# Performance work log

Hardware: AMD Instinct MI355X
Metric: run time of the kernel (lower is better)

The kernel has to match this reference:

```python
import jax, jax.numpy as jnp
import numpy as np

B, T, E, H = 8, 2048, 1024, 128


def setup_inputs() -> dict:
    key = jax.random.key(0)
    kx, kk, kq, kv = jax.random.split(key, 4)
    x = jax.random.normal(kx, (B, T, E), dtype=jnp.float32)
    # nn.Linear(E, H, bias=False) weights, stored as (E, H) so y = x @ W
    scale = 0.02
    Wk = jax.random.normal(kk, (E, H), dtype=jnp.float32) * scale
    Wq = jax.random.normal(kq, (E, H), dtype=jnp.float32) * scale
    Wv = jax.random.normal(kv, (E, H), dtype=jnp.float32) * scale
    return {"x": x, "Wk": Wk, "Wq": Wq, "Wv": Wv}


def reference(x, Wk, Wq, Wv):
    # x: (B,T,E) -> k,q,v: (B,T,H)
    k = x @ Wk
    q = x @ Wq
    v = x @ Wv
    # att[b,t,s] = q[b,t] . k[b,s]
    att = jnp.einsum('bth,bsh->bts', q, k)
    # original: att / head_norm, head_norm = 1/sqrt(H)  => multiply by sqrt(H)
    att = att * jnp.sqrt(jnp.float32(H))
    tril = jnp.tril(jnp.ones((T, T), dtype=bool))
    att = jnp.where(tril, att, -jnp.inf)
    # original softmax over dim=1 (query axis), NOT the key axis
    att = jax.nn.softmax(att, axis=1)
    return att @ v  # (B,T,H)
```

## Files before the change

### kernel.cpp

```cpp
#include <hip/hip_runtime.h>
#include <math.h>

#define Bn 8
#define Tn 2048
#define En 1024
#define Hn 128
#define SQRTH_LOG2E (11.313708498984761f * 1.4426950408889634f)

typedef __attribute__((ext_vector_type(8))) short short8;
typedef __attribute__((ext_vector_type(8))) _Float16 half8;
typedef __attribute__((ext_vector_type(4))) short short4v;
typedef __attribute__((ext_vector_type(4))) float float4v;

#define MFMA16(a, b, c)  __builtin_amdgcn_mfma_f32_16x16x32_bf16((a), (b), (c), 0, 0, 0)
#define MFMA16F(a, b, c) __builtin_amdgcn_mfma_f32_16x16x32_f16((a), (b), (c), 0, 0, 0)
#define EXP2(x) __builtin_amdgcn_exp2f(x)

static __device__ __forceinline__ unsigned short f2bf(float f) {
    unsigned u = __float_as_uint(f);
    u += 0x7FFFu + ((u >> 16) & 1u);
    return (unsigned short)(u >> 16);
}
static __device__ __forceinline__ unsigned short f2h(float f) {
    _Float16 h = (_Float16)f;
    union { _Float16 v; unsigned short u; } c; c.v = h; return c.u;
}

static __device__ __forceinline__ void gll16(const unsigned short* g, unsigned short* l) {
    __builtin_amdgcn_global_load_lds(
        (const __attribute__((address_space(1))) unsigned int*)g,
        (__attribute__((address_space(3))) unsigned int*)l, 16, 0, 0);
}


__global__ __launch_bounds__(256) void prep_kernel(
    const float* __restrict__ x,
    const float* __restrict__ Wq, const float* __restrict__ Wk, const float* __restrict__ Wv,
    unsigned short* __restrict__ xt, unsigned short* __restrict__ wtt)
{
    if (blockIdx.x < 8192) {
        int g = blockIdx.x * 256 + threadIdx.x;
        int kc8 = g & 3;
        int rr = (g >> 2) & 63;
        int ks = (g >> 8) & 31;
        int mt = g >> 13;
        size_t src = ((size_t)mt * 64 + rr) * En + ks * 32 + kc8 * 8;
        float4v f0 = *(const float4v*)(x + src);
        float4v f1 = *(const float4v*)(x + src + 4);
        short8 h;
#pragma unroll
        for (int j = 0; j < 4; j++) {
            h[j] = (short)f2h(f0[j]);
            h[j + 4] = (short)f2h(f1[j]);
        }
        size_t d = (size_t)(g >> 2) * 32 + (size_t)(kc8 ^ (rr & 3)) * 8;
        *(short8*)(xt + d) = h;
    } else {
        int t = (blockIdx.x - 8192) * 256 + threadIdx.x;
        int kc8 = t & 3;
        int hh = (t >> 2) & 127;
        int ks = (t >> 9) & 31;
        int z = t >> 14;
        const float* W = (z == 0) ? Wq : ((z == 1) ? Wk : Wv);
        short8 h8;
#pragma unroll
        for (int j = 0; j < 8; j++) {
            int e = ks * 32 + kc8 * 8 + j;
            h8[j] = (short)f2h(W[(size_t)e * Hn + hh]);
        }
        size_t d = (((size_t)z * 32 + ks) * 4096) + (size_t)hh * 32
                 + (size_t)(kc8 ^ (hh & 3)) * 8;
        *(short8*)(wtt + d) = h8;
    }
}

__global__ __launch_bounds__(256) void proj_kernel(
    const unsigned short* __restrict__ xt, const unsigned short* __restrict__ wtt,
    unsigned short* __restrict__ qf, unsigned short* __restrict__ kf,
    unsigned short* __restrict__ vtt)
{
    __shared__ __align__(16) unsigned short lds[2][6144];
    int z = blockIdx.y;
    int mt = blockIdx.x;
    int tid = threadIdx.x;
    int wave = tid >> 6, lane = tid & 63;
    int c15 = lane & 15, kg = lane >> 4;
    int sb = c15 & 3;
    int mrow = wave >> 1, ncol = wave & 1;

    const unsigned short* A0 = xt + (size_t)mt * 32 * 2048;
    const unsigned short* B0 = wtt + (size_t)z * 32 * 4096;

    float4v acc[2][4];
#pragma unroll
    for (int i = 0; i < 2; i++)
#pragma unroll
        for (int j = 0; j < 4; j++) acc[i][j] = (float4v)0.0f;

    const unsigned short* gcur[3];
    int lbo[3];
    int gstep[3];
#pragma unroll
    for (int i = 0; i < 3; i++) {
        int ch = wave * 3 + i;
        if (ch < 4) { gcur[i] = A0 + ch * 512;       lbo[i] = ch * 512;        gstep[i] = 2048; }
        else        { gcur[i] = B0 + (ch - 4) * 512; lbo[i] = 2048 + (ch - 4) * 512; gstep[i] = 4096; }
    }
    int lo8 = lane * 8;

    auto stage = [&](int buf) {
        unsigned short* Lb = lds[0] + buf * 6144;
#pragma unroll
        for (int i = 0; i < 3; i++) {
            gll16(gcur[i] + lo8, Lb + lbo[i] + lo8);
            gcur[i] += gstep[i];
        }
    };

    stage(0);

    for (int ks = 0; ks < 32; ks++) {
        __syncthreads();
        if (ks + 1 < 32) stage((ks + 1) & 1);
        const unsigned short* Lb = lds[ks & 1];

        half8 ah[2], bh[4];
#pragma unroll
        for (int mi = 0; mi < 2; mi++) {
            int row = mrow * 32 + mi * 16 + c15;
            ah[mi] = *(const half8*)(Lb + row * 32 + (kg ^ sb) * 8);
        }
#pragma unroll
        for (int ni = 0; ni < 4; ni++) {
            int row = ncol * 64 + ni * 16 + c15;
            bh[ni] = *(const half8*)(Lb + 2048 + row * 32 + (kg ^ sb) * 8);
        }
#pragma unroll
        for (int mi = 0; mi < 2; mi++)
#pragma unroll
            for (int ni = 0; ni < 4; ni++)
                acc[mi][ni] = MFMA16F(ah[mi], bh[ni], acc[mi][ni]);
    }

    if (z < 2) {
        unsigned short* oh = (z == 0) ? qf : kf;
#pragma unroll
        for (int mi = 0; mi < 2; mi++) {
#pragma unroll
            for (int ni = 0; ni < 4; ni++) {
                int h = ncol * 64 + ni * 16 + c15;
#pragma unroll
                for (int r = 0; r < 4; r++) {
                    int t = mt * 64 + mrow * 32 + mi * 16 + kg * 4 + r;
                    size_t o = (size_t)t * Hn + (((h >> 3) ^ (t & 15)) << 3) + (h & 7);
                    oh[o] = f2h(acc[mi][ni][r]);
                }
            }
        }
    } else {
        int b = mt >> 5;
#pragma unroll
        for (int mi = 0; mi < 2; mi++) {
            int t0 = (mt & 31) * 64 + mrow * 32 + mi * 16 + kg * 4;
            int sc = t0 >> 5, so = t0 & 31;
#pragma unroll
            for (int ni = 0; ni < 4; ni++) {
                int h = ncol * 64 + ni * 16 + c15;
                short4v pk;
#pragma unroll
                for (int r = 0; r < 4; r++) pk[r] = (short)f2bf(acc[mi][ni][r]);
                int so2 = ((((so >> 3) ^ ((h >> 1) & 3))) << 3) | (so & 7);
                *(short4v*)(vtt + (((size_t)b * 64 + sc) * 128 + h) * 32 + so2) = pk;
            }
        }
    }
}

__global__ __launch_bounds__(256) void stats_part_kernel(
    const unsigned short* __restrict__ qf, const unsigned short* __restrict__ kf,
    float* __restrict__ m_part, float* __restrict__ l_part)
{
    __shared__ __align__(16) unsigned short lds[4096];
    int tid = threadIdx.x;
    int wave = tid >> 6, lane = tid & 63;
    int c15 = lane & 15, kg = lane >> 4;
    int b = blockIdx.x;

    int rem = (int)blockIdx.y, sj, nch = 1;
    for (sj = 0; sj < 32; sj++) {
        nch = ((31 - sj) >> 2) + 1;
        if (rem < nch) break;
        rem -= nch;
    }
    int ci = rem;
    int c0 = 2 * sj;
    int len = 64 - c0;
    int cbase = len / nch, ext = len % nch;
    int cs = c0 + ci * cbase + (ci < ext ? ci : ext);
    int ce = cs + cbase + (ci < ext ? 1 : 0);

    int s_base = sj * 64 + wave * 16;

    half8 a[4];
    {
        int s = s_base + c15;
        const unsigned short* kr = kf + ((size_t)(b * Tn + s)) * Hn;
#pragma unroll
        for (int st = 0; st < 4; st++) {
            int off = ((st * 4 + kg) ^ c15) * 8;
            a[st] = *(const half8*)(kr + off);
        }
    }
    float m[4], l[4];
#pragma unroll
    for (int r = 0; r < 4; r++) { m[r] = -3.0e38f; l[r] = 0.0f; }

    auto stage = [&](int c) {
        const unsigned short* Qf = qf + ((size_t)b * Tn + c * 32) * Hn;
        int lo8 = lane * 8;
#pragma unroll
        for (int i = 0; i < 2; i++) {
            int ch = wave * 2 + i;
            gll16(Qf + ch * 512 + lo8, lds + ch * 512 + lo8);
        }
    };

    for (int c = cs; c < ce; c++) {
        stage(c);
        __syncthreads();
#pragma unroll
        for (int half = 0; half < 2; half++) {
            int t16 = c * 32 + half * 16;
            int tl = half * 16 + c15;
            float4v a1 = (float4v)0.0f;
#pragma unroll
            for (int st = 0; st < 4; st++) {
                int off = tl * 128 + ((st * 4 + kg) ^ c15) * 8;
                half8 bh = *(const half8*)(lds + off);
                a1 = MFMA16F(a[st], bh, a1);
            }
            int t = t16 + c15;
#pragma unroll
            for (int r = 0; r < 4; r++) {
                float attv = a1[r] * SQRTH_LOG2E;
                int s_row = s_base + kg * 4 + r;
                bool valid = (t >= s_row);
                float cand = valid ? attv : -3.0e38f;
                float mn = fmaxf(m[r], cand);
                l[r] = l[r] * EXP2(m[r] - mn) + (valid ? EXP2(attv - mn) : 0.0f);
                m[r] = mn;
            }
        }
        __syncthreads();
    }
#pragma unroll
    for (int mask = 1; mask < 16; mask <<= 1) {
#pragma unroll
        for (int r = 0; r < 4; r++) {
            float mo = __shfl_xor(m[r], mask);
            float lo2 = __shfl_xor(l[r], mask);
            float mn = fmaxf(m[r], mo);
            l[r] = l[r] * EXP2(m[r] - mn) + lo2 * EXP2(mo - mn);
            m[r] = mn;
        }
    }
    if (c15 == 0) {
#pragma unroll
        for (int r = 0; r < 4; r++) {
            int sl = wave * 16 + kg * 4 + r;
            size_t d = ((((size_t)b * 32 + sj) * 8 + ci) * 64) + sl;
            m_part[d] = m[r];
            l_part[d] = l[r];
        }
    }
}

__global__ __launch_bounds__(256) void stats_combine_kernel(
    const float* __restrict__ m_part, const float* __restrict__ l_part,
    float2* __restrict__ ml_st)
{
    int g = blockIdx.x * 256 + threadIdx.x;
    int s = g & 2047, b = g >> 11;
    int sj = s >> 6, sl = s & 63;
    int nch = ((31 - sj) >> 2) + 1;
    size_t base = (((size_t)b * 32 + sj) * 8) * 64 + sl;
    float M = m_part[base];
    float L = l_part[base];
    for (int ci = 1; ci < nch; ci++) {
        float mi = m_part[base + (size_t)ci * 64];
        float li = l_part[base + (size_t)ci * 64];
        float mn = fmaxf(M, mi);
        L = L * EXP2(M - mn) + li * EXP2(mi - mn);
        M = mn;
    }
    float2 ml; ml.x = M; ml.y = 1.0f / L;
    ml_st[(size_t)b * Tn + s] = ml;
}

__global__ __launch_bounds__(256) void out_part_kernel(
    const unsigned short* __restrict__ qf, const unsigned short* __restrict__ kf,
    const unsigned short* __restrict__ vtt,
    const float2* __restrict__ ml_st,
    float* __restrict__ part_out)
{
    __shared__ __align__(16) unsigned short lds[8192];
    __shared__ __align__(16) unsigned short pbuf[4][16][40];
    int tid = threadIdx.x;
    int wave = tid >> 6, lane = tid & 63;
    int c15 = lane & 15, kg = lane >> 4;
    int b = blockIdx.x;

    int rem = (int)blockIdx.y, tj, nch = 1;
    for (tj = 31; tj >= 0; tj--) {
        nch = (tj >> 2) + 1;
        if (rem < nch) break;
        rem -= nch;
    }
    int ci = rem;
    int len = 2 * tj + 2;
    int cbase = len / nch, ext = len % nch;
    int cs = ci * cbase + (ci < ext ? ci : ext);
    int ce = cs + cbase + (ci < ext ? 1 : 0);

    int t_base = tj * 64 + wave * 16;

    half8 qa[4];
    {
        int t = t_base + c15;
        const unsigned short* qr = qf + ((size_t)(b * Tn + t)) * Hn;
#pragma unroll
        for (int st = 0; st < 4; st++) {
            int off = ((st * 4 + kg) ^ c15) * 8;
            qa[st] = *(const half8*)(qr + off);
        }
    }
    float4v oacc[8];
#pragma unroll
    for (int i = 0; i < 8; i++) oacc[i] = (float4v)0.0f;

    auto stage = [&](int c) {
        const unsigned short* Kf = kf + ((size_t)b * Tn + c * 32) * Hn;
        const unsigned short* Vv = vtt + ((size_t)b * 64 + c) * (128 * 32);
        int lo8 = lane * 8;
#pragma unroll
        for (int i = 0; i < 4; i++) {
            int ch = wave * 4 + i;
            const unsigned short* g;
            unsigned short* ld;
            if (ch < 8) { g = Kf + ch * 512;       ld = lds + ch * 512; }
            else        { g = Vv + (ch - 8) * 512; ld = lds + 4096 + (ch - 8) * 512; }
            gll16(g + lo8, ld + lo8);
        }
    };

    for (int c = cs; c < ce; c++) {
        stage(c);
        __syncthreads();
#pragma unroll
        for (int half = 0; half < 2; half++) {
            int s16 = c * 32 + half * 16;
            int sl = half * 16 + c15;
            float4v a1 = (float4v)0.0f;
#pragma unroll
            for (int st = 0; st < 4; st++) {
                int off = sl * 128 + ((st * 4 + kg) ^ c15) * 8;
                half8 bh = *(const half8*)(lds + off);
                a1 = MFMA16F(qa[st], bh, a1);
            }
            float2 mlv = ml_st[b * Tn + s16 + c15];
#pragma unroll
            for (int r = 0; r < 4; r++) {
                int t = t_base + kg * 4 + r;
                float attv = a1[r] * SQRTH_LOG2E;
                float earg = fminf(attv - mlv.x, 0.0f);
                float p = (t >= s16 + c15) ? EXP2(earg) * mlv.y : 0.0f;
                pbuf[wave][kg * 4 + r][c15 + half * 16] = f2bf(p);
            }
        }
        short8 pa = *(const short8*)&pbuf[wave][c15][kg * 8];
#pragma unroll
        for (int nt = 0; nt < 8; nt++) {
            int voff = (nt * 16 + c15) * 32 + ((kg ^ ((c15 >> 1) & 3)) * 8);
            short8 vb = *(const short8*)(lds + 4096 + voff);
            oacc[nt] = MFMA16(pa, vb, oacc[nt]);
        }
        __syncthreads();
    }
    float* po = part_out + ((((size_t)b * 32 + tj) * 8 + ci) * 64) * 128;
#pragma unroll
    for (int nt = 0; nt < 8; nt++) {
        int h = nt * 16 + c15;
#pragma unroll
        for (int r = 0; r < 4; r++) {
            int tl = wave * 16 + kg * 4 + r;
            po[(size_t)tl * 128 + h] = oacc[nt][r];
        }
    }
}

__global__ __launch_bounds__(256) void out_combine_kernel(
    const float* __restrict__ part_out, float* __restrict__ out)
{
    int g = blockIdx.x * 256 + threadIdx.x;
    int h4 = g & 31;
    int t = (g >> 5) & 2047;
    int b = g >> 16;
    int tj = t >> 6, tl = t & 63;
    int nch = (tj >> 2) + 1;
    const float4v* p = (const float4v*)(part_out
        + ((((size_t)b * 32 + tj) * 8) * 64 + tl) * 128) + h4;
    float4v acc = p[0];
    for (int ci = 1; ci < nch; ci++) acc += p[(size_t)ci * 2048];
    *((float4v*)(out + ((size_t)b * Tn + t) * Hn) + h4) = acc;
}

extern "C" void kernel_launch(void* const* d_in, const int* in_sizes, int n_in,
                              void* d_out, int out_size, void* d_ws, size_t ws_size,
                              hipStream_t stream)
{
    (void)in_sizes; (void)n_in; (void)out_size; (void)ws_size;
    const float* x  = (const float*)d_in[0];
    const float* Wk = (const float*)d_in[1];
    const float* Wq = (const float*)d_in[2];
    const float* Wv = (const float*)d_in[3];
    float* out = (float*)d_out;

    const size_t NQ = (size_t)Bn * Tn * Hn;
    const size_t NX = (size_t)Bn * Tn * En;
    unsigned short* qf  = (unsigned short*)d_ws;
    unsigned short* qlo = qf + NQ;
    unsigned short* kf  = qlo + NQ;
    unsigned short* klo = kf + NQ;
    unsigned short* vtt  = klo + NQ;
    unsigned short* xt   = vtt + NQ;
    unsigned short* xt_lo = xt + NX;
    unsigned short* wtt  = xt_lo + NX;
    unsigned short* wtt_lo = wtt + (size_t)3 * Hn * En;
    float2* ml_st = (float2*)(wtt_lo + (size_t)3 * Hn * En);

    float* part_out = (float*)xt;
    float* m_part   = (float*)wtt;
    float* l_part   = (float*)wtt_lo;

    prep_kernel<<<dim3(8384), 256, 0, stream>>>(x, Wq, Wk, Wv, xt, wtt);
    proj_kernel<<<dim3(256, 3), 256, 0, stream>>>(xt, wtt, qf, kf, vtt);
    stats_part_kernel<<<dim3(Bn, 144), 256, 0, stream>>>(qf, kf, m_part, l_part);
    stats_combine_kernel<<<dim3(64), 256, 0, stream>>>(m_part, l_part, ml_st);
    out_part_kernel<<<dim3(Bn, 144), 256, 0, stream>>>(qf, kf, vtt,
                                                       ml_st, part_out);
    out_combine_kernel<<<dim3(2048), 256, 0, stream>>>(part_out, out);
}
```

Before: 174.2 us.

## Fuse stats combine into output kernel and batch online-softmax updates

Result: faster. 169.3 us (median of 2 runs) (-2.8%).

```diff
diff --git a/kernel.cpp b/kernel.cpp
--- a/kernel.cpp
+++ b/kernel.cpp
@@ -228,9 +228,9 @@
     for (int c = cs; c < ce; c++) {
         stage(c);
         __syncthreads();
+        float4v av[2];
 #pragma unroll
         for (int half = 0; half < 2; half++) {
-            int t16 = c * 32 + half * 16;
             int tl = half * 16 + c15;
             float4v a1 = (float4v)0.0f;
 #pragma unroll
@@ -239,17 +239,23 @@
                 half8 bh = *(const half8*)(lds + off);
                 a1 = MFMA16F(a[st], bh, a1);
             }
-            int t = t16 + c15;
-#pragma unroll
-            for (int r = 0; r < 4; r++) {
-                float attv = a1[r] * SQRTH_LOG2E;
-                int s_row = s_base + kg * 4 + r;
-                bool valid = (t >= s_row);
-                float cand = valid ? attv : -3.0e38f;
-                float mn = fmaxf(m[r], cand);
-                l[r] = l[r] * EXP2(m[r] - mn) + (valid ? EXP2(attv - mn) : 0.0f);
-                m[r] = mn;
-            }
+            av[half] = a1;
+        }
+        int t0 = c * 32 + c15;
+        int t1 = c * 32 + 16 + c15;
+#pragma unroll
+        for (int r = 0; r < 4; r++) {
+            int s_row = s_base + kg * 4 + r;
+            float v0 = av[0][r] * SQRTH_LOG2E;
+            float v1 = av[1][r] * SQRTH_LOG2E;
+            bool val0 = (t0 >= s_row), val1 = (t1 >= s_row);
+            float c0v = val0 ? v0 : -3.0e38f;
+            float c1v = val1 ? v1 : -3.0e38f;
+            float mn = fmaxf(m[r], fmaxf(c0v, c1v));
+            l[r] = l[r] * EXP2(m[r] - mn)
+                 + (val0 ? EXP2(v0 - mn) : 0.0f)
+                 + (val1 ? EXP2(v1 - mn) : 0.0f);
+            m[r] = mn;
         }
         __syncthreads();
     }
@@ -275,36 +281,15 @@
     }
 }
 
-__global__ __launch_bounds__(256) void stats_combine_kernel(
-    const float* __restrict__ m_part, const float* __restrict__ l_part,
-    float2* __restrict__ ml_st)
-{
-    int g = blockIdx.x * 256 + threadIdx.x;
-    int s = g & 2047, b = g >> 11;
-    int sj = s >> 6, sl = s & 63;
-    int nch = ((31 - sj) >> 2) + 1;
-    size_t base = (((size_t)b * 32 + sj) * 8) * 64 + sl;
-    float M = m_part[base];
-    float L = l_part[base];
-    for (int ci = 1; ci < nch; ci++) {
-        float mi = m_part[base + (size_t)ci * 64];
-        float li = l_part[base + (size_t)ci * 64];
-        float mn = fmaxf(M, mi);
-        L = L * EXP2(M - mn) + li * EXP2(mi - mn);
-        M = mn;
-    }
-    float2 ml; ml.x = M; ml.y = 1.0f / L;
-    ml_st[(size_t)b * Tn + s] = ml;
-}
-
 __global__ __launch_bounds__(256) void out_part_kernel(
     const unsigned short* __restrict__ qf, const unsigned short* __restrict__ kf,
     const unsigned short* __restrict__ vtt,
-    const float2* __restrict__ ml_st,
+    const float* __restrict__ m_part, const float* __restrict__ l_part,
     float* __restrict__ part_out)
 {
     __shared__ __align__(16) unsigned short lds[8192];
     __shared__ __align__(16) unsigned short pbuf[4][16][40];
+    __shared__ float2 mlbuf[256];
     int tid = threadIdx.x;
     int wave = tid >> 6, lane = tid & 63;
     int c15 = lane & 15, kg = lane >> 4;
@@ -321,6 +306,27 @@
     int cbase = len / nch, ext = len % nch;
     int cs = ci * cbase + (ci < ext ? ci : ext);
     int ce = cs + cbase + (ci < ext ? 1 : 0);
+
+    {
+        int ncols = (ce - cs) * 32;
+        if (tid < ncols) {
+            int s = cs * 32 + tid;
+            int sj2 = s >> 6, sl2 = s & 63;
+            int nchs = ((31 - sj2) >> 2) + 1;
+            size_t base = (((size_t)b * 32 + sj2) * 8) * 64 + sl2;
+            float M = m_part[base];
+            float L = l_part[base];
+            for (int cj = 1; cj < nchs; cj++) {
+                float mi = m_part[base + (size_t)cj * 64];
+                float li = l_part[base + (size_t)cj * 64];
+                float mn = fmaxf(M, mi);
+                L = L * EXP2(M - mn) + li * EXP2(mi - mn);
+                M = mn;
+            }
+            float2 ml; ml.x = M; ml.y = 1.0f / L;
+            mlbuf[tid] = ml;
+        }
+    }
 
     int t_base = tj * 64 + wave * 16;
 
@@ -367,7 +373,7 @@
                 half8 bh = *(const half8*)(lds + off);
                 a1 = MFMA16F(qa[st], bh, a1);
             }
-            float2 mlv = ml_st[b * Tn + s16 + c15];
+            float2 mlv = mlbuf[(c - cs) * 32 + sl];
 #pragma unroll
             for (int r = 0; r < 4; r++) {
                 int t = t_base + kg * 4 + r;
@@ -436,7 +442,6 @@
     unsigned short* xt_lo = xt + NX;
     unsigned short* wtt  = xt_lo + NX;
     unsigned short* wtt_lo = wtt + (size_t)3 * Hn * En;
-    float2* ml_st = (float2*)(wtt_lo + (size_t)3 * Hn * En);
 
     float* part_out = (float*)xt;
     float* m_part   = (float*)wtt;
@@ -445,8 +450,7 @@
     prep_kernel<<<dim3(8384), 256, 0, stream>>>(x, Wq, Wk, Wv, xt, wtt);
     proj_kernel<<<dim3(256, 3), 256, 0, stream>>>(xt, wtt, qf, kf, vtt);
     stats_part_kernel<<<dim3(Bn, 144), 256, 0, stream>>>(qf, kf, m_part, l_part);
-    stats_combine_kernel<<<dim3(64), 256, 0, stream>>>(m_part, l_part, ml_st);
     out_part_kernel<<<dim3(Bn, 144), 256, 0, stream>>>(qf, kf, vtt,
-                                                       ml_st, part_out);
+                                                       m_part, l_part, part_out);
     out_combine_kernel<<<dim3(2048), 256, 0, stream>>>(part_out, out);
 }
```
